# Kernel optimization log

Hardware: AMD Instinct MI355X
Metric: run time of the kernel (lower is better)

Reference implementation:

```python
import jax, jax.numpy as jnp
import numpy as np

N_FFT = 800
HOP = 200
WIN = 800
FREQ = N_FFT // 2 + 1  # 401
B, T = 32, 480000


def _make_weights():
    # periodic hann window
    n = np.arange(N_FFT)
    window = 0.5 - 0.5 * np.cos(2.0 * np.pi * np.arange(WIN) / WIN)
    k = np.arange(FREQ)
    angle = 2.0 * np.pi * np.outer(k, n) / N_FFT  # [FREQ, N_FFT]
    fwd_real = (np.cos(angle) * window).astype(np.float32)
    fwd_imag = (-np.sin(angle) * window).astype(np.float32)
    angle_t = 2.0 * np.pi * np.outer(n, k) / N_FFT  # [N_FFT, FREQ]
    inv_window = window * (1.0 / N_FFT)
    bwd_real = (np.cos(angle_t).T * inv_window).astype(np.float32)  # [FREQ, N_FFT]
    bwd_imag = (np.sin(angle_t).T * inv_window).astype(np.float32)
    return (jnp.asarray(fwd_real), jnp.asarray(fwd_imag),
            jnp.asarray(bwd_real), jnp.asarray(bwd_imag))


def setup_inputs() -> dict:
    key = jax.random.key(0)
    x = jax.random.normal(key, (B, T), dtype=jnp.float32)
    wfr, wfi, wbr, wbi = _make_weights()
    return {"x": x, "w_fwd_real": wfr, "w_fwd_imag": wfi,
            "w_bwd_real": wbr, "w_bwd_imag": wbi}


def reference(x, w_fwd_real, w_fwd_imag, w_bwd_real, w_bwd_imag):
    Tlen = x.shape[-1]
    pad = N_FFT // 2
    xp = jnp.pad(x, ((0, 0), (pad, pad)), mode="edge")  # replicate pad
    n_frames = (xp.shape[-1] - N_FFT) // HOP + 1
    # frame extraction (== conv1d stride HOP with dense DFT kernels)
    fidx = jnp.arange(n_frames)[:, None] * HOP + jnp.arange(N_FFT)[None, :]
    frames = xp[:, fidx]  # [B, F, N_FFT]
    real = jnp.einsum("bfn,kn->bkf", frames, w_fwd_real)  # [B, FREQ, F]
    imag = jnp.einsum("bfn,kn->bkf", frames, w_fwd_imag)
    magnitude = jnp.sqrt(real * real + imag * imag + 1e-14)
    phase = jnp.arctan2(imag, real)
    phase = jnp.where((imag == 0) & (real < 0), jnp.pi, phase)
    # inverse: iDFT-as-GEMM + overlap-add (== conv_transpose1d stride HOP)
    rp = magnitude * jnp.cos(phase)
    ip = magnitude * jnp.sin(phase)
    yr = jnp.einsum("bkf,kn->bfn", rp, w_bwd_real)  # [B, F, N_FFT]
    yi = jnp.einsum("bkf,kn->bfn", ip, w_bwd_imag)
    y_frames = yr - yi
    l_out = (n_frames - 1) * HOP + N_FFT
    oidx = jnp.arange(n_frames)[:, None] * HOP + jnp.arange(N_FFT)[None, :]
    wave = jnp.zeros((x.shape[0], l_out), dtype=x.dtype).at[:, oidx].add(y_frames)
    return wave[:, pad:pad + Tlen]
```

## Files before the change

### kernel.cpp

```cpp
#include <hip/hip_runtime.h>
#include <math.h>

#define HOP     200
#define NB      32
#define TLEN    480000
#define NSEGT   2400
#define WSEG    10
#define WPS     (WSEG + 6)
#define NWT     (NSEGT / WSEG)
#define WPB     4
#define NBLKX   (NWT / WPB)

#define DLT  0.00785398163397448f
#define C1K  0.99996915760f
#define S1K  0.00785390090f
#define C2K  0.99987663248f
#define S2K  0.01570731731f
#define C3K  0.99972243010f
#define S3K  0.02355976470f
#define C40  0.95105651629515f
#define S40  0.30901699437495f

typedef float floatx4 __attribute__((ext_vector_type(4)));

#define WSYNC() asm volatile("s_waitcnt lgkmcnt(0)" ::: "memory")

__global__ __launch_bounds__(256) void stft_wave(const float* __restrict__ x,
                                                 float* __restrict__ out) {
    __shared__ float  part[WPB][WPS][10][6];
    __shared__ float  pg[WPB][WPS][6];
    __shared__ float4 segc[WPB][2][WSEG];

    const int w    = threadIdx.x >> 6;
    const int lane = threadIdx.x & 63;
    const int b    = blockIdx.y;
    const int wt   = blockIdx.x * WPB + w;
    const int wq0  = wt * WSEG;
    const float* xb = x + (size_t)b * TLEN;

    for (int u = lane; u < WPS * 10; u += 64) {
        const int s = u / 10;
        const int k = u - 10 * s;
        const int g = wq0 - 3 + s;
        const int gm = (g + 4) & 3;
        float c0, sn0;
        __sincosf((float)(gm * 200 + 4 * k) * DLT, &sn0, &c0);

        float4 v[5];
        if (g >= 0 && g <= 2399) {
            const float4* xs = (const float4*)(xb + 200 * g);
#pragma unroll
            for (int i = 0; i < 5; ++i) v[i] = xs[k + 10 * i];
        } else {
            const float e = (g < 0) ? xb[0] : xb[TLEN - 1];
#pragma unroll
            for (int i = 0; i < 5; ++i) v[i] = make_float4(e, e, e, e);
        }

        float p1e = 0.f, p1o = 0.f, pce = 0.f, pco = 0.f, pse = 0.f, pso = 0.f;
#pragma unroll
        for (int i = 0; i < 5; ++i) {
            const float c1 = c0 * C1K - sn0 * S1K, s1 = sn0 * C1K + c0 * S1K;
            const float c2 = c0 * C2K - sn0 * S2K, s2 = sn0 * C2K + c0 * S2K;
            const float c3 = c0 * C3K - sn0 * S3K, s3 = sn0 * C3K + c0 * S3K;
            p1e += v[i].x + v[i].z;             p1o += v[i].y + v[i].w;
            pce += c0 * v[i].x + c2 * v[i].z;   pco += c1 * v[i].y + c3 * v[i].w;
            pse += sn0 * v[i].x + s2 * v[i].z;  pso += s1 * v[i].y + s3 * v[i].w;
            const float cn = c0 * C40 - sn0 * S40;
            sn0 = sn0 * C40 + c0 * S40;  c0 = cn;
        }
        part[w][s][k][0] = p1e;  part[w][s][k][1] = p1o;
        part[w][s][k][2] = pce;  part[w][s][k][3] = pco;
        part[w][s][k][4] = pse;  part[w][s][k][5] = pso;
    }
    WSYNC();

    for (int u = lane; u < WPS * 6; u += 64) {
        const int s = u / 6;
        const int c = u - 6 * s;
        float a = 0.f;
#pragma unroll
        for (int k = 0; k < 10; ++k) a += part[w][s][k][c];
        pg[w][s][c] = a;
    }
    WSYNC();

    if (lane < 2 * WSEG) {
        const int par = lane & 1;
        const int ql  = lane >> 1;
        const int q   = wq0 + ql;
        float A = 0.f, C = 0.f, D = 0.f;
#pragma unroll
        for (int df = -1; df <= 2; ++df) {
            const int f = q + df;
            if (f < 0 || f > 2400) continue;
            const int ls0 = f - wq0 + 1;
            float sp1 = 0.f, spc = 0.f, sps = 0.f;
#pragma unroll
            for (int kk = 0; kk < 4; ++kk) {
                const float* rec = pg[w][ls0 + kk];
                sp1 += rec[par];  spc += rec[2 + par];  sps += rec[4 + par];
            }
            const int fm = f & 3;
            const float tr = (fm == 0) ? spc : (fm == 1) ? sps : (fm == 2) ? -spc : -sps;
            const float S = 0.5f * sp1 + 0.5f * tr;
            A += S;
            if (fm == 0) C += S; else if (fm == 2) C -= S;
            else if (fm == 1) D += S; else D -= S;
        }
        segc[w][par][ql] = make_float4(A * (1.0f / 1600.0f),
                                       sqrtf(C * C + D * D) * (1.0f / 1600.0f),
                                       atan2f(D, C), 0.f);
    }
    WSYNC();

    const bool headw = (wq0 == 0);
    const bool tailw = (wq0 + WSEG == NSEGT);
    const float4* xg4 = (const float4*)xb + 50 * wq0;
    floatx4* og4 = (floatx4*)(out + (size_t)b * TLEN) + 50 * wq0;
    const int pmb = (wq0 & 3) * 200 + 400;
    for (int j = lane; j < 50 * WSEG; j += 64) {
        const float4 xv = xg4[j];
        const int sl = j / 50;
        const float4 ce = segc[w][0][sl];
        const float4 co = segc[w][1][sl];
        const int pm = (pmb + 4 * j) % 800;
        const float xa[4] = {xv.x, xv.y, xv.z, xv.w};
        float r[4];
#pragma unroll
        for (int c = 0; c < 4; ++c) {
            const float4 cc = (c & 1) ? co : ce;
            r[c] = 0.75f * xa[c] + cc.x - cc.y * __cosf((float)(pm + c) * DLT - cc.z);
        }
        if (headw && sl == 0) {
#pragma unroll
            for (int c = 0; c < 4; ++c) {
                const float wm = 0.5f + 0.5f * __sinf((float)(pm + c) * DLT);
                r[c] -= 0.5f * wm * wm * xa[c];
            }
        }
        if (tailw && sl == WSEG - 1) {
#pragma unroll
            for (int c = 0; c < 4; ++c) {
                const float wm = 0.5f - 0.5f * __sinf((float)(pm + c) * DLT);
                r[c] -= 0.5f * wm * wm * xa[c];
            }
        }
        floatx4 rv = {r[0], r[1], r[2], r[3]};
        __builtin_nontemporal_store(rv, &og4[j]);
    }
}

extern "C" void kernel_launch(void* const* d_in, const int* in_sizes, int n_in,
                              void* d_out, int out_size, void* d_ws, size_t ws_size,
                              hipStream_t stream) {
    const float* x = (const float*)d_in[0];
    float* out = (float*)d_out;
    stft_wave<<<dim3(NBLKX, NB), dim3(256), 0, stream>>>(x, out);
}
```

Measured before the change: 128.4 us.

## Process three tiles per wave, overlapping next-tile analysis with current output

Each wavefront now handles three consecutive 10-segment tiles instead of one. The per-segment partial DFT sums for the next tile are interleaved with the output loop of the current tile, so the loads for the next tile can overlap the output arithmetic and stores. The block size drops to 128 threads and the grid shrinks. This gives fewer resident waves for hiding memory latency and adds a serial dependency chain within each wave.

```diff
diff --git a/kernel.cpp b/kernel.cpp
--- a/kernel.cpp
+++ b/kernel.cpp
@@ -7,9 +7,10 @@
 #define NSEGT   2400
 #define WSEG    10
 #define WPS     (WSEG + 6)
-#define NWT     (NSEGT / WSEG)
-#define WPB     4
-#define NBLKX   (NWT / WPB)
+#define NTPW    3
+#define WPB     2
+#define PWR     (NSEGT / (WSEG * NTPW))
+#define NBLKX   (PWR / WPB)
 
 #define DLT  0.00785398163397448f
 #define C1K  0.99996915760f
@@ -25,23 +26,24 @@
 
 #define WSYNC() asm volatile("s_waitcnt lgkmcnt(0)" ::: "memory")
 
-__global__ __launch_bounds__(256) void stft_wave(const float* __restrict__ x,
+__global__ __launch_bounds__(128) void stft_pipe(const float* __restrict__ x,
                                                  float* __restrict__ out) {
     __shared__ float  part[WPB][WPS][10][6];
     __shared__ float  pg[WPB][WPS][6];
     __shared__ float4 segc[WPB][2][WSEG];
 
-    const int w    = threadIdx.x >> 6;
-    const int lane = threadIdx.x & 63;
-    const int b    = blockIdx.y;
-    const int wt   = blockIdx.x * WPB + w;
-    const int wq0  = wt * WSEG;
+    const int w     = threadIdx.x >> 6;
+    const int lane  = threadIdx.x & 63;
+    const int b     = blockIdx.y;
+    const int pw    = blockIdx.x * WPB + w;
+    const int tbase = pw * NTPW;
     const float* xb = x + (size_t)b * TLEN;
-
-    for (int u = lane; u < WPS * 10; u += 64) {
+    float* ob       = out + (size_t)b * TLEN;
+
+    auto A_item = [&](int q0, int u) {
         const int s = u / 10;
         const int k = u - 10 * s;
-        const int g = wq0 - 3 + s;
+        const int g = q0 - 3 + s;
         const int gm = (g + 4) & 3;
         float c0, sn0;
         __sincosf((float)(gm * 200 + 4 * k) * DLT, &sn0, &c0);
@@ -72,59 +74,54 @@
         part[w][s][k][0] = p1e;  part[w][s][k][1] = p1o;
         part[w][s][k][2] = pce;  part[w][s][k][3] = pco;
         part[w][s][k][4] = pse;  part[w][s][k][5] = pso;
-    }
-    WSYNC();
-
-    for (int u = lane; u < WPS * 6; u += 64) {
-        const int s = u / 6;
-        const int c = u - 6 * s;
-        float a = 0.f;
-#pragma unroll
-        for (int k = 0; k < 10; ++k) a += part[w][s][k][c];
-        pg[w][s][c] = a;
-    }
-    WSYNC();
-
-    if (lane < 2 * WSEG) {
-        const int par = lane & 1;
-        const int ql  = lane >> 1;
-        const int q   = wq0 + ql;
-        float A = 0.f, C = 0.f, D = 0.f;
-#pragma unroll
-        for (int df = -1; df <= 2; ++df) {
-            const int f = q + df;
-            if (f < 0 || f > 2400) continue;
-            const int ls0 = f - wq0 + 1;
-            float sp1 = 0.f, spc = 0.f, sps = 0.f;
-#pragma unroll
-            for (int kk = 0; kk < 4; ++kk) {
-                const float* rec = pg[w][ls0 + kk];
-                sp1 += rec[par];  spc += rec[2 + par];  sps += rec[4 + par];
-            }
-            const int fm = f & 3;
-            const float tr = (fm == 0) ? spc : (fm == 1) ? sps : (fm == 2) ? -spc : -sps;
-            const float S = 0.5f * sp1 + 0.5f * tr;
-            A += S;
-            if (fm == 0) C += S; else if (fm == 2) C -= S;
-            else if (fm == 1) D += S; else D -= S;
-        }
-        segc[w][par][ql] = make_float4(A * (1.0f / 1600.0f),
-                                       sqrtf(C * C + D * D) * (1.0f / 1600.0f),
-                                       atan2f(D, C), 0.f);
-    }
-    WSYNC();
-
-    const bool headw = (wq0 == 0);
-    const bool tailw = (wq0 + WSEG == NSEGT);
-    const float4* xg4 = (const float4*)xb + 50 * wq0;
-    floatx4* og4 = (floatx4*)(out + (size_t)b * TLEN) + 50 * wq0;
-    const int pmb = (wq0 & 3) * 200 + 400;
-    for (int j = lane; j < 50 * WSEG; j += 64) {
-        const float4 xv = xg4[j];
+    };
+
+    auto phaseB = [&]() {
+        for (int u = lane; u < WPS * 6; u += 64) {
+            const int s = u / 6;
+            const int c = u - 6 * s;
+            float a = 0.f;
+#pragma unroll
+            for (int k = 0; k < 10; ++k) a += part[w][s][k][c];
+            pg[w][s][c] = a;
+        }
+    };
+
+    auto phaseC = [&](int q0) {
+        if (lane < 2 * WSEG) {
+            const int par = lane & 1;
+            const int ql  = lane >> 1;
+            const int q   = q0 + ql;
+            float A = 0.f, C = 0.f, D = 0.f;
+#pragma unroll
+            for (int df = -1; df <= 2; ++df) {
+                const int f = q + df;
+                if (f < 0 || f > 2400) continue;
+                const int ls0 = f - q0 + 1;
+                float sp1 = 0.f, spc = 0.f, sps = 0.f;
+#pragma unroll
+                for (int kk = 0; kk < 4; ++kk) {
+                    const float* rec = pg[w][ls0 + kk];
+                    sp1 += rec[par];  spc += rec[2 + par];  sps += rec[4 + par];
+                }
+                const int fm = f & 3;
+                const float tr = (fm == 0) ? spc : (fm == 1) ? sps : (fm == 2) ? -spc : -sps;
+                const float S = 0.5f * sp1 + 0.5f * tr;
+                A += S;
+                if (fm == 0) C += S; else if (fm == 2) C -= S;
+                else if (fm == 1) D += S; else D -= S;
+            }
+            segc[w][par][ql] = make_float4(A * (1.0f / 1600.0f),
+                                           sqrtf(C * C + D * D) * (1.0f / 1600.0f),
+                                           atan2f(D, C), 0.f);
+        }
+    };
+
+    auto D_comp = [&](int q0, int j, const float4& xv, bool headw, bool tailw) {
         const int sl = j / 50;
         const float4 ce = segc[w][0][sl];
         const float4 co = segc[w][1][sl];
-        const int pm = (pmb + 4 * j) % 800;
+        const int pm = (((q0 & 3) * 200 + 400) + 4 * j) % 800;
         const float xa[4] = {xv.x, xv.y, xv.z, xv.w};
         float r[4];
 #pragma unroll
@@ -147,7 +144,50 @@
             }
         }
         floatx4 rv = {r[0], r[1], r[2], r[3]};
-        __builtin_nontemporal_store(rv, &og4[j]);
+        __builtin_nontemporal_store(rv, (floatx4*)ob + 50 * q0 + j);
+    };
+
+    {
+        const int q0 = tbase * WSEG;
+        for (int u = lane; u < WPS * 10; u += 64) A_item(q0, u);
+        WSYNC();
+        phaseB();
+        WSYNC();
+        phaseC(q0);
+        WSYNC();
+    }
+
+    for (int tt = 0; tt < NTPW; ++tt) {
+        const int t  = tbase + tt;
+        const int q0 = t * WSEG;
+        const bool headw = (q0 == 0);
+        const bool tailw = (q0 + WSEG == NSEGT);
+
+        if (tt + 1 < NTPW) {
+            const int q2 = q0 + WSEG;
+#pragma unroll
+            for (int kk = 0; kk < 8; ++kk) {
+                const int j = lane + 64 * kk;
+                const bool dj = (j < 50 * WSEG);
+                float4 xv;
+                if (dj) xv = ((const float4*)xb)[50 * q0 + j];
+                if ((kk & 1) == 0 && kk < 6) {
+                    const int u = lane + 64 * (kk >> 1);
+                    if (u < WPS * 10) A_item(q2, u);
+                }
+                if (dj) D_comp(q0, j, xv, headw, tailw);
+            }
+            WSYNC();
+            phaseB();
+            WSYNC();
+            phaseC(q2);
+            WSYNC();
+        } else {
+            for (int j = lane; j < 50 * WSEG; j += 64) {
+                const float4 xv = ((const float4*)xb)[50 * q0 + j];
+                D_comp(q0, j, xv, headw, tailw);
+            }
+        }
     }
 }
 
@@ -156,5 +196,5 @@
                               hipStream_t stream) {
     const float* x = (const float*)d_in[0];
     float* out = (float*)d_out;
-    stft_wave<<<dim3(NBLKX, NB), dim3(256), 0, stream>>>(x, out);
+    stft_pipe<<<dim3(NBLKX, NB), dim3(128), 0, stream>>>(x, out);
 }
```

After: 132.0 us. +2.8%, slower.

## Split block into producer/consumer waves with ring buffer of segment partials

Applied to the files above, without the earlier changes.

Restructures each block to process six consecutive 10-segment tiles. Two waves produce per-segment partial sums into a shared ring buffer while the other two waves compute the segment coefficients and write the output, separated by block barriers. Adjacent tiles reuse the ring-buffer partials, so the 6-segment halo is no longer recomputed for every tile. The output pass swaps per-element __cosf and atan2/sqrt for a rotation recurrence in C/D form. The cost is a barrier every stage, only half the waves doing each kind of work, and fewer blocks in the grid.

```diff
diff --git a/kernel.cpp b/kernel.cpp
--- a/kernel.cpp
+++ b/kernel.cpp
@@ -6,10 +6,10 @@
 #define TLEN    480000
 #define NSEGT   2400
 #define WSEG    10
-#define WPS     (WSEG + 6)
 #define NWT     (NSEGT / WSEG)
-#define WPB     4
-#define NBLKX   (NWT / WPB)
+#define NTPB    6
+#define NBLKX   (NWT / NTPB)
+#define RING    32
 
 #define DLT  0.00785398163397448f
 #define C1K  0.99996915760f
@@ -20,134 +20,167 @@
 #define S3K  0.02355976470f
 #define C40  0.95105651629515f
 #define S40  0.30901699437495f
+#define C512 -0.63742398974869f
+#define S512 -0.77051324277579f
 
 typedef float floatx4 __attribute__((ext_vector_type(4)));
 
 #define WSYNC() asm volatile("s_waitcnt lgkmcnt(0)" ::: "memory")
+#define LBAR()  asm volatile("s_waitcnt lgkmcnt(0)\n\ts_barrier" ::: "memory")
 
-__global__ __launch_bounds__(256) void stft_wave(const float* __restrict__ x,
-                                                 float* __restrict__ out) {
-    __shared__ float  part[WPB][WPS][10][6];
-    __shared__ float  pg[WPB][WPS][6];
-    __shared__ float4 segc[WPB][2][WSEG];
+__global__ __launch_bounds__(256) void stft_pc(const float* __restrict__ x,
+                                               float* __restrict__ out) {
+    __shared__ float  part[2][8][10][6];
+    __shared__ float  pg[RING][6];
+    __shared__ float4 segc[2][2][WSEG];
 
     const int w    = threadIdx.x >> 6;
     const int lane = threadIdx.x & 63;
     const int b    = blockIdx.y;
-    const int wt   = blockIdx.x * WPB + w;
-    const int wq0  = wt * WSEG;
+    const int bt0  = blockIdx.x * NTPB;
     const float* xb = x + (size_t)b * TLEN;
+    float* ob       = out + (size_t)b * TLEN;
 
-    for (int u = lane; u < WPS * 10; u += 64) {
-        const int s = u / 10;
-        const int k = u - 10 * s;
-        const int g = wq0 - 3 + s;
-        const int gm = (g + 4) & 3;
-        float c0, sn0;
-        __sincosf((float)(gm * 200 + 4 * k) * DLT, &sn0, &c0);
+    auto produce = [&](int g0, int nrh) {
+        const int nb_ = w * nrh;
+        for (int u = lane; u < nrh * 10; u += 64) {
+            const int nl = u / 10;
+            const int k  = u - 10 * nl;
+            const int g  = g0 + nb_ + nl;
+            const int gm = (g + 4) & 3;
+            float c0, sn0;
+            __sincosf((float)(gm * 200 + 4 * k) * DLT, &sn0, &c0);
 
-        float4 v[5];
-        if (g >= 0 && g <= 2399) {
-            const float4* xs = (const float4*)(xb + 200 * g);
+            float4 v[5];
+            if (g >= 0 && g <= 2399) {
+                const float4* xs = (const float4*)(xb + 200 * g);
 #pragma unroll
-            for (int i = 0; i < 5; ++i) v[i] = xs[k + 10 * i];
+                for (int i = 0; i < 5; ++i) v[i] = xs[k + 10 * i];
+            } else {
+                const float e = (g < 0) ? xb[0] : xb[TLEN - 1];
+#pragma unroll
+                for (int i = 0; i < 5; ++i) v[i] = make_float4(e, e, e, e);
+            }
+
+            float p1e = 0.f, p1o = 0.f, pce = 0.f, pco = 0.f, pse = 0.f, pso = 0.f;
+#pragma unroll
+            for (int i = 0; i < 5; ++i) {
+                const float c1 = c0 * C1K - sn0 * S1K, s1 = sn0 * C1K + c0 * S1K;
+                const float c2 = c0 * C2K - sn0 * S2K, s2 = sn0 * C2K + c0 * S2K;
+                const float c3 = c0 * C3K - sn0 * S3K, s3 = sn0 * C3K + c0 * S3K;
+                p1e += v[i].x + v[i].z;             p1o += v[i].y + v[i].w;
+                pce += c0 * v[i].x + c2 * v[i].z;   pco += c1 * v[i].y + c3 * v[i].w;
+                pse += sn0 * v[i].x + s2 * v[i].z;  pso += s1 * v[i].y + s3 * v[i].w;
+                const float cn = c0 * C40 - sn0 * S40;
+                sn0 = sn0 * C40 + c0 * S40;  c0 = cn;
+            }
+            part[w][nl][k][0] = p1e;  part[w][nl][k][1] = p1o;
+            part[w][nl][k][2] = pce;  part[w][nl][k][3] = pco;
+            part[w][nl][k][4] = pse;  part[w][nl][k][5] = pso;
+        }
+        WSYNC();
+        for (int u = lane; u < nrh * 6; u += 64) {
+            const int nl = u / 6;
+            const int c  = u - 6 * nl;
+            float a = 0.f;
+#pragma unroll
+            for (int k = 0; k < 10; ++k) a += part[w][nl][k][c];
+            pg[(g0 + nb_ + nl + RING) & (RING - 1)][c] = a;
+        }
+    };
+
+    auto phaseC = [&](int tl) {
+        const int cid = threadIdx.x & 127;
+        if (cid < 2 * WSEG) {
+            const int q0  = (bt0 + tl) * WSEG;
+            const int par = cid & 1;
+            const int ql  = cid >> 1;
+            const int q   = q0 + ql;
+            float A = 0.f, C = 0.f, D = 0.f;
+#pragma unroll
+            for (int df = -1; df <= 2; ++df) {
+                const int f = q + df;
+                if (f < 0 || f > 2400) continue;
+                float sp1 = 0.f, spc = 0.f, sps = 0.f;
+#pragma unroll
+                for (int kk = 0; kk < 4; ++kk) {
+                    const float* rec = pg[(f - 2 + kk + RING) & (RING - 1)];
+                    sp1 += rec[par];  spc += rec[2 + par];  sps += rec[4 + par];
+                }
+                const int fm = f & 3;
+                const float tr = (fm == 0) ? spc : (fm == 1) ? sps : (fm == 2) ? -spc : -sps;
+                const float S = 0.5f * sp1 + 0.5f * tr;
+                A += S;
+                if (fm == 0) C += S; else if (fm == 2) C -= S;
+                else if (fm == 1) D += S; else D -= S;
+            }
+            segc[tl & 1][par][ql] = make_float4(A * (1.0f / 1600.0f),
+                                                C * (1.0f / 1600.0f),
+                                                D * (1.0f / 1600.0f), 0.f);
+        }
+    };
+
+    auto phaseD = [&](int tl) {
+        const int cid = threadIdx.x & 127;
+        const int tg  = bt0 + tl;
+        const int q0  = tg * WSEG;
+        const int buf = tl & 1;
+        const bool headw = (tg == 0);
+        const bool tailw = (tg == NWT - 1);
+        const float4* xg4 = (const float4*)xb + 50 * q0;
+        floatx4* og4 = (floatx4*)ob + 50 * q0;
+        const int pmb = (q0 & 3) * 200 + 400;
+
+        float cf, sf;
+        __sincosf((float)(pmb + 4 * cid) * DLT, &sf, &cf);
+#pragma unroll
+        for (int m = 0; m < 4; ++m) {
+            const int j = cid + 128 * m;
+            if (j < 50 * WSEG) {
+                const float4 xv = xg4[j];
+                const int sl = j / 50;
+                const float4 e = segc[buf][0][sl];
+                const float4 o = segc[buf][1][sl];
+                const float c1f = cf * C1K - sf * S1K, s1f = sf * C1K + cf * S1K;
+                const float c2f = cf * C2K - sf * S2K, s2f = sf * C2K + cf * S2K;
+                const float c3f = cf * C3K - sf * S3K, s3f = sf * C3K + cf * S3K;
+                float r0 = 0.75f * xv.x + e.x - (e.y * cf  + e.z * sf);
+                float r1 = 0.75f * xv.y + o.x - (o.y * c1f + o.z * s1f);
+                float r2 = 0.75f * xv.z + e.x - (e.y * c2f + e.z * s2f);
+                float r3 = 0.75f * xv.w + o.x - (o.y * c3f + o.z * s3f);
+                if (headw && sl == 0) {
+                    const float w0 = 0.5f + 0.5f * sf,  w1 = 0.5f + 0.5f * s1f;
+                    const float w2 = 0.5f + 0.5f * s2f, w3 = 0.5f + 0.5f * s3f;
+                    r0 -= 0.5f * w0 * w0 * xv.x;  r1 -= 0.5f * w1 * w1 * xv.y;
+                    r2 -= 0.5f * w2 * w2 * xv.z;  r3 -= 0.5f * w3 * w3 * xv.w;
+                }
+                if (tailw && sl == WSEG - 1) {
+                    const float w0 = 0.5f - 0.5f * sf,  w1 = 0.5f - 0.5f * s1f;
+                    const float w2 = 0.5f - 0.5f * s2f, w3 = 0.5f - 0.5f * s3f;
+                    r0 -= 0.5f * w0 * w0 * xv.x;  r1 -= 0.5f * w1 * w1 * xv.y;
+                    r2 -= 0.5f * w2 * w2 * xv.z;  r3 -= 0.5f * w3 * w3 * xv.w;
+                }
+                floatx4 rv = {r0, r1, r2, r3};
+                __builtin_nontemporal_store(rv, &og4[j]);
+            }
+            const float cn = cf * C512 - sf * S512;
+            sf = sf * C512 + cf * S512;  cf = cn;
+        }
+    };
+
+    for (int s = -1; s <= NTPB; ++s) {
+        if (w < 2) {
+            const int tp = s + 1;
+            if (tp == 0) {
+                produce(bt0 * WSEG - 3, 8);
+            } else if (tp < NTPB) {
+                produce((bt0 + tp) * WSEG + 3, 5);
+            }
         } else {
-            const float e = (g < 0) ? xb[0] : xb[TLEN - 1];
-#pragma unroll
-            for (int i = 0; i < 5; ++i) v[i] = make_float4(e, e, e, e);
+            if (s >= 0 && s < NTPB) phaseC(s);
+            if (s >= 1)             phaseD(s - 1);
         }
-
-        float p1e = 0.f, p1o = 0.f, pce = 0.f, pco = 0.f, pse = 0.f, pso = 0.f;
-#pragma unroll
-        for (int i = 0; i < 5; ++i) {
-            const float c1 = c0 * C1K - sn0 * S1K, s1 = sn0 * C1K + c0 * S1K;
-            const float c2 = c0 * C2K - sn0 * S2K, s2 = sn0 * C2K + c0 * S2K;
-            const float c3 = c0 * C3K - sn0 * S3K, s3 = sn0 * C3K + c0 * S3K;
-            p1e += v[i].x + v[i].z;             p1o += v[i].y + v[i].w;
-            pce += c0 * v[i].x + c2 * v[i].z;   pco += c1 * v[i].y + c3 * v[i].w;
-            pse += sn0 * v[i].x + s2 * v[i].z;  pso += s1 * v[i].y + s3 * v[i].w;
-            const float cn = c0 * C40 - sn0 * S40;
-            sn0 = sn0 * C40 + c0 * S40;  c0 = cn;
-        }
-        part[w][s][k][0] = p1e;  part[w][s][k][1] = p1o;
-        part[w][s][k][2] = pce;  part[w][s][k][3] = pco;
-        part[w][s][k][4] = pse;  part[w][s][k][5] = pso;
-    }
-    WSYNC();
-
-    for (int u = lane; u < WPS * 6; u += 64) {
-        const int s = u / 6;
-        const int c = u - 6 * s;
-        float a = 0.f;
-#pragma unroll
-        for (int k = 0; k < 10; ++k) a += part[w][s][k][c];
-        pg[w][s][c] = a;
-    }
-    WSYNC();
-
-    if (lane < 2 * WSEG) {
-        const int par = lane & 1;
-        const int ql  = lane >> 1;
-        const int q   = wq0 + ql;
-        float A = 0.f, C = 0.f, D = 0.f;
-#pragma unroll
-        for (int df = -1; df <= 2; ++df) {
-            const int f = q + df;
-            if (f < 0 || f > 2400) continue;
-            const int ls0 = f - wq0 + 1;
-            float sp1 = 0.f, spc = 0.f, sps = 0.f;
-#pragma unroll
-            for (int kk = 0; kk < 4; ++kk) {
-                const float* rec = pg[w][ls0 + kk];
-                sp1 += rec[par];  spc += rec[2 + par];  sps += rec[4 + par];
-            }
-            const int fm = f & 3;
-            const float tr = (fm == 0) ? spc : (fm == 1) ? sps : (fm == 2) ? -spc : -sps;
-            const float S = 0.5f * sp1 + 0.5f * tr;
-            A += S;
-            if (fm == 0) C += S; else if (fm == 2) C -= S;
-            else if (fm == 1) D += S; else D -= S;
-        }
-        segc[w][par][ql] = make_float4(A * (1.0f / 1600.0f),
-                                       sqrtf(C * C + D * D) * (1.0f / 1600.0f),
-                                       atan2f(D, C), 0.f);
-    }
-    WSYNC();
-
-    const bool headw = (wq0 == 0);
-    const bool tailw = (wq0 + WSEG == NSEGT);
-    const float4* xg4 = (const float4*)xb + 50 * wq0;
-    floatx4* og4 = (floatx4*)(out + (size_t)b * TLEN) + 50 * wq0;
-    const int pmb = (wq0 & 3) * 200 + 400;
-    for (int j = lane; j < 50 * WSEG; j += 64) {
-        const float4 xv = xg4[j];
-        const int sl = j / 50;
-        const float4 ce = segc[w][0][sl];
-        const float4 co = segc[w][1][sl];
-        const int pm = (pmb + 4 * j) % 800;
-        const float xa[4] = {xv.x, xv.y, xv.z, xv.w};
-        float r[4];
-#pragma unroll
-        for (int c = 0; c < 4; ++c) {
-            const float4 cc = (c & 1) ? co : ce;
-            r[c] = 0.75f * xa[c] + cc.x - cc.y * __cosf((float)(pm + c) * DLT - cc.z);
-        }
-        if (headw && sl == 0) {
-#pragma unroll
-            for (int c = 0; c < 4; ++c) {
-                const float wm = 0.5f + 0.5f * __sinf((float)(pm + c) * DLT);
-                r[c] -= 0.5f * wm * wm * xa[c];
-            }
-        }
-        if (tailw && sl == WSEG - 1) {
-#pragma unroll
-            for (int c = 0; c < 4; ++c) {
-                const float wm = 0.5f - 0.5f * __sinf((float)(pm + c) * DLT);
-                r[c] -= 0.5f * wm * wm * xa[c];
-            }
-        }
-        floatx4 rv = {r[0], r[1], r[2], r[3]};
-        __builtin_nontemporal_store(rv, &og4[j]);
+        LBAR();
     }
 }
 
@@ -156,5 +189,5 @@
                               hipStream_t stream) {
     const float* x = (const float*)d_in[0];
     float* out = (float*)d_out;
-    stft_wave<<<dim3(NBLKX, NB), dim3(256), 0, stream>>>(x, out);
+    stft_pc<<<dim3(NBLKX, NB), dim3(256), 0, stream>>>(x, out);
 }
```

Result: faster. 124.7 us (-2.9%).
